# Performance work log

Measured on AMD Instinct MI355X. Metric: run time of the kernel, lower is better.

Reference implementation:

```python
import jax, jax.numpy as jnp
import numpy as np

N, E, F, HID, HEADS, L, B, R = 50000, 400000, 64, 256, 4, 4, 16, 8
C = HID // HEADS  # per-head channels = 64
LN_EPS = 1e-5
NEG_SLOPE = 0.2  # GATConv LeakyReLU default


def _posenc(n, d):
    pos = jnp.arange(n, dtype=jnp.float32)[:, None]
    i = jnp.arange(d, dtype=jnp.float32)[None, :]
    rates = 1.0 / 10000.0 ** (2.0 * jnp.floor(i / 2.0) / d)
    ang = pos * rates
    return jnp.where(jnp.arange(d)[None, :] % 2 == 0, jnp.sin(ang), jnp.cos(ang))


def _layernorm(x, g, b):
    mu = x.mean(-1, keepdims=True)
    var = ((x - mu) ** 2).mean(-1, keepdims=True)
    return (x - mu) * jax.lax.rsqrt(var + LN_EPS) * g + b


def _gat_layer(x, src, dst, W, a_src, a_dst, bias):
    # x: [N, HID]; W: [HID, HID]; a_src/a_dst: [HEADS, C]; bias: [HID]
    h = (x @ W).reshape(N, HEADS, C)
    s_src = (h * a_src[None]).sum(-1)  # [N, HEADS]
    s_dst = (h * a_dst[None]).sum(-1)  # [N, HEADS]
    e = jax.nn.leaky_relu(s_src[src] + s_dst[dst], NEG_SLOPE)  # [E', HEADS]
    m = jax.ops.segment_max(e, dst, num_segments=N)
    ex = jnp.exp(e - m[dst])
    denom = jax.ops.segment_sum(ex, dst, num_segments=N)
    alpha = ex / denom[dst]  # softmax over incoming edges per dst node
    out = jax.ops.segment_sum(alpha[:, :, None] * h[src], dst, num_segments=N)
    return out.reshape(N, HID) + bias


def setup_inputs() -> dict:
    key = jax.random.key(0)
    ks = jax.random.split(key, 20)
    sc = 0.05
    batch = jnp.sort(jax.random.randint(ks[2], (N,), 0, B))
    return {
        "x": jax.random.normal(ks[0], (N, F), jnp.float32),
        "region_emb_w": jax.random.normal(ks[3], (R, F), jnp.float32) * sc,
        "in_proj_w": jax.random.normal(ks[4], (3 * F, HID), jnp.float32) * sc,
        "in_proj_b": jnp.zeros((HID,), jnp.float32),
        "gat_w": jax.random.normal(ks[5], (L, HID, HID), jnp.float32) * sc,
        "att_src": jax.random.normal(ks[6], (L, HEADS, C), jnp.float32) * sc,
        "att_dst": jax.random.normal(ks[7], (L, HEADS, C), jnp.float32) * sc,
        "gat_b": jnp.zeros((L, HID), jnp.float32),
        "ln_g": jnp.ones((L, HID), jnp.float32),
        "ln_b": jnp.zeros((L, HID), jnp.float32),
        "ro_w1": jax.random.normal(ks[8], (HID, HID), jnp.float32) * sc,
        "ro_b1": jnp.zeros((HID,), jnp.float32),
        "ro_w2": jax.random.normal(ks[9], (HID, HID), jnp.float32) * sc,
        "ro_b2": jnp.zeros((HID,), jnp.float32),
        "edge_index": jax.random.randint(ks[1], (2, E), 0, N),
        "batch": batch,
        "region_ids": jax.random.randint(ks[10], (N,), 0, R),
    }


def reference(x, region_emb_w, in_proj_w, in_proj_b, gat_w, att_src, att_dst,
              gat_b, ln_g, ln_b, ro_w1, ro_b1, ro_w2, ro_b2,
              edge_index, batch, region_ids):
    # input features: x | region embedding | sinusoidal posenc  -> [N, 3F]
    feats = jnp.concatenate([x, region_emb_w[region_ids], _posenc(N, F)], axis=-1)
    h = feats @ in_proj_w + in_proj_b
    # add self loops once (GATConv add_self_loops=True)
    loop = jnp.arange(N)
    src = jnp.concatenate([edge_index[0], loop])
    dst = jnp.concatenate([edge_index[1], loop])
    for l in range(L):
        h = _gat_layer(h, src, dst, gat_w[l], att_src[l], att_dst[l], gat_b[l])
        h = _layernorm(jax.nn.relu(h), ln_g[l], ln_b[l])
        # dropout is identity in eval mode
    # global mean pool over graphs
    sums = jax.ops.segment_sum(h, batch, num_segments=B)
    cnts = jax.ops.segment_sum(jnp.ones((N,), h.dtype), batch, num_segments=B)
    pooled = sums / jnp.maximum(cnts, 1.0)[:, None]  # [B, HID]
    out = jax.nn.gelu(pooled @ ro_w1 + ro_b1, approximate=False) @ ro_w2 + ro_b2
    return out
```

## Files before the change

### kernel.cpp

```cpp
#include <hip/hip_runtime.h>
#include <cmath>

typedef unsigned short u16;
typedef unsigned char u8;
typedef unsigned int u32;
typedef short bf16x8 __attribute__((ext_vector_type(8)));
typedef float f32x4 __attribute__((ext_vector_type(4)));
typedef float f32x2 __attribute__((ext_vector_type(2)));

#define NN 50000
#define MP 50048
#define EE 400000
#define ET 450000
#define HIDD 256
#define KIN 192
#define LN_EPSF 1e-5f

__device__ __forceinline__ float bf2f(u16 u){ return __uint_as_float(((u32)u)<<16); }
__device__ __forceinline__ u16 f2bf(float f){
  u32 x = __float_as_uint(f);
  u32 r = x + 0x7fffu + ((x>>16)&1u);
  return (u16)(r>>16);
}
__device__ __forceinline__ u32 pack2(float a, float b){ return (u32)f2bf(a) | ((u32)f2bf(b)<<16); }
__device__ __forceinline__ u8 f2fp8(float v){
  return (u8)(__builtin_amdgcn_cvt_pk_fp8_f32(v, v, 0, false) & 0xff);
}

__device__ __forceinline__ void dma16(const u16* g, u16* lds){
  __builtin_amdgcn_global_load_lds(
      (const __attribute__((address_space(1))) void*)g,
      (__attribute__((address_space(3))) void*)lds, 16, 0, 0);
}

__global__ __launch_bounds__(256) void k_setup(
    const float* __restrict__ x, const float* __restrict__ remb, const int* __restrict__ rid,
    u16* __restrict__ feats,
    const float* __restrict__ ipw, const float* __restrict__ gatw,
    u16* __restrict__ wtin, u16* __restrict__ wtl,
    const float* __restrict__ asrc, const float* __restrict__ adst, u16* __restrict__ vmat,
    const int* __restrict__ ei, int* __restrict__ deg)
{
  int b = blockIdx.x;
  if (b < 12512){
    int e = b*768 + threadIdx.x;
    #pragma unroll
    for (int it=0; it<3; ++it, e+=256){
      int n = e / 192;
      int c = e - n*192;
      if (n >= MP) break;
      float v = 0.f;
      if (n < NN){
        if (c < 64){
          v = x[n*64 + c];
        } else if (c < 128){
          v = remb[rid[n]*64 + (c-64)];
        } else {
          int i = c - 128;
          float rate = exp2f(-(float)(2*(i>>1)) * (1.0f/64.0f) * 13.287712379549449f);
          float s, cc;
          __sincosf((float)n * rate, &s, &cc);
          v = (i & 1) ? cc : s;
        }
      }
      feats[(size_t)n*192 + c] = f2bf(v);
    }
  } else if (b < 13728){
    int idx = (b - 12512)*256 + threadIdx.x;
    if (idx < 49152){
      int n = idx / 192, k = idx - n*192;
      wtin[idx] = f2bf(ipw[k*256 + n]);
    } else {
      int j = idx - 49152;
      if (j < 262144){
        int l = j >> 16, rem = j & 65535;
        int n = rem >> 8, k = rem & 255;
        wtl[j] = f2bf(gatw[l*65536 + k*256 + n]);
      }
    }
  } else if (b < 13792){
    int idx = (b - 13728)*256 + threadIdx.x;
    if (idx < 16384){
      int l = idx >> 12, rem = idx & 4095, v = rem >> 8, k = rem & 255;
      float s = 0.f;
      if (v < 8){
        const float* a = (v < 4) ? (asrc + l*256 + v*64) : (adst + l*256 + (v-4)*64);
        const float* w = gatw + (size_t)l*65536 + k*256 + (v & 3)*64;
        #pragma unroll 8
        for (int c=0;c<64;++c) s += w[c]*a[c];
      }
      vmat[idx] = f2bf(s);
    }
  } else {
    int i = (b - 13792)*256 + threadIdx.x;
    if (i < ET){
      int d = (i < EE) ? ei[EE + i] : (i - EE);
      atomicAdd(&deg[d], 1);
    }
  }
}

__global__ void k_scan1(const int* __restrict__ deg, int* __restrict__ row_off, int* __restrict__ part){
  __shared__ int s[256];
  int n = blockIdx.x*256 + threadIdx.x;
  int v = (n < NN) ? deg[n] : 0;
  s[threadIdx.x] = v;
  __syncthreads();
  for (int off=1; off<256; off<<=1){
    int t = (threadIdx.x >= off) ? s[threadIdx.x - off] : 0;
    __syncthreads();
    s[threadIdx.x] += t;
    __syncthreads();
  }
  if (n < NN) row_off[n] = s[threadIdx.x] - v;
  if (threadIdx.x == 255) part[blockIdx.x] = s[255];
}

__global__ void k_scan23(int* __restrict__ row_off, const int* __restrict__ part, int nparts){
  __shared__ int sp[256];
  int t = threadIdx.x;
  sp[t] = (t < nparts && t < (int)blockIdx.x) ? part[t] : 0;
  __syncthreads();
  for (int off=128; off; off>>=1){
    if (t < off) sp[t] += sp[t+off];
    __syncthreads();
  }
  int n = blockIdx.x*256 + t;
  if (n < NN) row_off[n] += sp[0];
}

__global__ void k_scatter(const int* __restrict__ ei, const int* __restrict__ row_off,
                          int* __restrict__ cur, int* __restrict__ csr_src){
  int i = blockIdx.x*blockDim.x + threadIdx.x;
  if (i >= ET) return;
  int s, d;
  if (i < EE){ s = ei[i]; d = ei[EE + i]; } else { s = i - EE; d = i - EE; }
  int pos = row_off[d] + atomicAdd(&cur[d], 1);
  csr_src[pos] = s;
}

template<int K>
__global__ __launch_bounds__(256, 3) void k_gemm(
    const u16* __restrict__ A, const u16* __restrict__ Wt,
    const float* __restrict__ bias, const u16* __restrict__ vmat,
    float* __restrict__ ss, float* __restrict__ sd,
    u16* __restrict__ C, u8* __restrict__ C8, int M)
{
  __shared__ u16 Asl[2][128*32];
  __shared__ u16 Bsl[2][128*32];
  int tid = threadIdx.x;
  int wave = tid >> 6, lane = tid & 63, quad = lane >> 4, lm = lane & 15;
  int r0 = blockIdx.x * 128;
  int cb = blockIdx.y;
  int rW = (wave >> 1) * 64;
  int cW = (wave & 1) * 64;
  bool doScore = vmat && (cb == 0) && ((wave & 1) == 0);

  f32x4 acc[4][4] = {};
  f32x4 accs[4] = {};

  auto stage = [&](int buf, int k0){
    for (int m = wave; m < 8; m += 4){
      int s = m*64 + lane;
      int r = s >> 2, p = s & 3;
      int c = p ^ ((r >> 2) & 3);
      dma16(A + (size_t)(r0 + r)*K + k0 + c*8, &Asl[buf][m*512]);
    }
    for (int m = wave; m < 8; m += 4){
      int s = m*64 + lane;
      int r = s >> 2, p = s & 3;
      int c = p ^ ((r >> 2) & 3);
      dma16(Wt + (size_t)(cb*128 + r)*K + k0 + c*8, &Bsl[buf][m*512]);
    }
  };

  stage(0, 0);
  __syncthreads();

  for (int ks = 0; ks < K/32; ++ks){
    int cur = ks & 1;
    if (ks + 1 < K/32) stage(cur ^ 1, (ks+1)*32);

    bf16x8 a[4], b[4];
    #pragma unroll
    for (int i=0;i<4;++i){
      int row = rW + i*16 + lm;
      int slot = row*4 + (quad ^ ((row >> 2) & 3));
      a[i] = *(const bf16x8*)(&Asl[cur][slot*8]);
    }
    #pragma unroll
    for (int j=0;j<4;++j){
      int row = cW + j*16 + lm;
      int slot = row*4 + (quad ^ ((row >> 2) & 3));
      b[j] = *(const bf16x8*)(&Bsl[cur][slot*8]);
    }
    #pragma unroll
    for (int i=0;i<4;++i)
      #pragma unroll
      for (int j=0;j<4;++j)
        acc[i][j] = __builtin_amdgcn_mfma_f32_16x16x32_bf16(a[i], b[j], acc[i][j], 0, 0, 0);
    if (doScore){
      bf16x8 bs = *(const bf16x8*)(vmat + (size_t)lm*K + ks*32 + quad*8);
      #pragma unroll
      for (int i=0;i<4;++i)
        accs[i] = __builtin_amdgcn_mfma_f32_16x16x32_bf16(a[i], bs, accs[i], 0, 0, 0);
    }
    __syncthreads();
  }

  if (doScore){
    #pragma unroll
    for (int i=0;i<4;++i){
      #pragma unroll
      for (int r=0;r<4;++r){
        int row = r0 + rW + i*16 + quad*4 + r;
        if (row < M){
          if (lm < 4)      ss[row*4 + lm]     = accs[i][r];
          else if (lm < 8) sd[row*4 + lm - 4] = accs[i][r];
        }
      }
    }
  }

  #pragma unroll
  for (int i=0;i<4;++i){
    #pragma unroll
    for (int r=0;r<4;++r){
      int row = r0 + rW + i*16 + quad*4 + r;
      if (row < M){
        #pragma unroll
        for (int j=0;j<4;++j){
          int col = cb*128 + cW + j*16 + lm;
          float v = acc[i][j][r];
          if (bias) v += bias[col];
          if (C)  C[(size_t)row*256 + col] = f2bf(v);
          if (C8) C8[(size_t)row*256 + col] = f2fp8(v);
        }
      }
    }
  }
}

__global__ __launch_bounds__(256) void k_aggregate(
    const u8* __restrict__ h8, const float* __restrict__ ssrc, const float* __restrict__ sdst,
    const int* __restrict__ row_off, const int* __restrict__ deg, const int* __restrict__ csr_src,
    const float* __restrict__ bias, const float* __restrict__ g, const float* __restrict__ bb,
    u16* __restrict__ hout, u8* __restrict__ hout8)
{
  int wv = (blockIdx.x*blockDim.x + threadIdx.x) >> 6;
  int lane = threadIdx.x & 63;
  int half = lane >> 5;
  int hl = lane & 31;
  int n = wv*2 + half;
  if (n >= NN) return;
  int c0 = hl*8;
  int head = hl >> 3;
  float sdh = sdst[n*4 + head];
  int ro = row_off[n];
  int dg = deg[n];
  float denA = 0.f, denB = 0.f;
  float a0=0,a1=0,a2=0,a3=0,a4=0,a5=0,a6=0,a7=0;
  float b0=0,b1=0,b2=0,b3=0,b4=0,b5=0,b6=0,b7=0;
  int j = 0;
  for (; j + 2 <= dg; j += 2){
    int sA = csr_src[ro+j];
    int sB = csr_src[ro+j+1];
    uint2 uA = *(const uint2*)(h8 + (size_t)sA*HIDD + c0);
    uint2 uB = *(const uint2*)(h8 + (size_t)sB*HIDD + c0);
    float eA = ssrc[sA*4+head] + sdh;
    float eB = ssrc[sB*4+head] + sdh;
    eA = (eA > 0.f) ? eA : 0.2f*eA;
    eB = (eB > 0.f) ? eB : 0.2f*eB;
    float xA = __expf(eA), xB = __expf(eB);
    denA += xA; denB += xB;
    f32x2 pA0 = __builtin_amdgcn_cvt_pk_f32_fp8((int)uA.x, false);
    f32x2 pA1 = __builtin_amdgcn_cvt_pk_f32_fp8((int)uA.x, true);
    f32x2 pA2 = __builtin_amdgcn_cvt_pk_f32_fp8((int)uA.y, false);
    f32x2 pA3 = __builtin_amdgcn_cvt_pk_f32_fp8((int)uA.y, true);
    f32x2 pB0 = __builtin_amdgcn_cvt_pk_f32_fp8((int)uB.x, false);
    f32x2 pB1 = __builtin_amdgcn_cvt_pk_f32_fp8((int)uB.x, true);
    f32x2 pB2 = __builtin_amdgcn_cvt_pk_f32_fp8((int)uB.y, false);
    f32x2 pB3 = __builtin_amdgcn_cvt_pk_f32_fp8((int)uB.y, true);
    a0 += xA*pA0.x; a1 += xA*pA0.y; a2 += xA*pA1.x; a3 += xA*pA1.y;
    a4 += xA*pA2.x; a5 += xA*pA2.y; a6 += xA*pA3.x; a7 += xA*pA3.y;
    b0 += xB*pB0.x; b1 += xB*pB0.y; b2 += xB*pB1.x; b3 += xB*pB1.y;
    b4 += xB*pB2.x; b5 += xB*pB2.y; b6 += xB*pB3.x; b7 += xB*pB3.y;
  }
  if (j < dg){
    int sA = csr_src[ro+j];
    uint2 uA = *(const uint2*)(h8 + (size_t)sA*HIDD + c0);
    float eA = ssrc[sA*4+head] + sdh;
    eA = (eA > 0.f) ? eA : 0.2f*eA;
    float xA = __expf(eA);
    denA += xA;
    f32x2 pA0 = __builtin_amdgcn_cvt_pk_f32_fp8((int)uA.x, false);
    f32x2 pA1 = __builtin_amdgcn_cvt_pk_f32_fp8((int)uA.x, true);
    f32x2 pA2 = __builtin_amdgcn_cvt_pk_f32_fp8((int)uA.y, false);
    f32x2 pA3 = __builtin_amdgcn_cvt_pk_f32_fp8((int)uA.y, true);
    a0 += xA*pA0.x; a1 += xA*pA0.y; a2 += xA*pA1.x; a3 += xA*pA1.y;
    a4 += xA*pA2.x; a5 += xA*pA2.y; a6 += xA*pA3.x; a7 += xA*pA3.y;
  }
  float inv = 1.f / (denA + denB);
  float y[8];
  y[0]=a0+b0; y[1]=a1+b1; y[2]=a2+b2; y[3]=a3+b3;
  y[4]=a4+b4; y[5]=a5+b5; y[6]=a6+b6; y[7]=a7+b7;
  float4 bi0 = *(const float4*)(bias + c0);
  float4 bi1 = *(const float4*)(bias + c0 + 4);
  y[0]=fmaxf(y[0]*inv+bi0.x,0.f); y[1]=fmaxf(y[1]*inv+bi0.y,0.f);
  y[2]=fmaxf(y[2]*inv+bi0.z,0.f); y[3]=fmaxf(y[3]*inv+bi0.w,0.f);
  y[4]=fmaxf(y[4]*inv+bi1.x,0.f); y[5]=fmaxf(y[5]*inv+bi1.y,0.f);
  y[6]=fmaxf(y[6]*inv+bi1.z,0.f); y[7]=fmaxf(y[7]*inv+bi1.w,0.f);
  float sum = (y[0]+y[1])+(y[2]+y[3])+((y[4]+y[5])+(y[6]+y[7]));
  #pragma unroll
  for (int o=16;o>=1;o>>=1) sum += __shfl_xor(sum, o);
  float mu = sum * (1.f/256.f);
  float d[8], sq = 0.f;
  #pragma unroll
  for (int k=0;k<8;++k){ d[k] = y[k]-mu; sq += d[k]*d[k]; }
  #pragma unroll
  for (int o=16;o>=1;o>>=1) sq += __shfl_xor(sq, o);
  float rs = rsqrtf(sq*(1.f/256.f) + LN_EPSF);
  float4 g0 = *(const float4*)(g + c0);
  float4 g1 = *(const float4*)(g + c0 + 4);
  float4 q0 = *(const float4*)(bb + c0);
  float4 q1 = *(const float4*)(bb + c0 + 4);
  float o0 = d[0]*rs*g0.x + q0.x, o1 = d[1]*rs*g0.y + q0.y;
  float o2 = d[2]*rs*g0.z + q0.z, o3 = d[3]*rs*g0.w + q0.w;
  float o4v= d[4]*rs*g1.x + q1.x, o5 = d[5]*rs*g1.y + q1.y;
  float o6 = d[6]*rs*g1.z + q1.z, o7 = d[7]*rs*g1.w + q1.w;
  if (hout8){
    u32 w0 = (u32)__builtin_amdgcn_cvt_pk_fp8_f32(o0, o1, 0, false);
    w0 = (u32)__builtin_amdgcn_cvt_pk_fp8_f32(o2, o3, (int)w0, true);
    u32 w1 = (u32)__builtin_amdgcn_cvt_pk_fp8_f32(o4v, o5, 0, false);
    w1 = (u32)__builtin_amdgcn_cvt_pk_fp8_f32(o6, o7, (int)w1, true);
    uint2 o8; o8.x = w0; o8.y = w1;
    *(uint2*)(hout8 + (size_t)n*HIDD + c0) = o8;
  } else {
    uint4 o4;
    o4.x = pack2(o0, o1);
    o4.y = pack2(o2, o3);
    o4.z = pack2(o4v, o5);
    o4.w = pack2(o6, o7);
    *(uint4*)(hout + (size_t)n*HIDD + c0) = o4;
  }
}

__global__ __launch_bounds__(256) void k_pool(
    const u8* __restrict__ h8, const int* __restrict__ batch,
    float* __restrict__ pooled, float* __restrict__ cnt)
{
  const int chunk = 25;
  int t = threadIdx.x;
  int n0 = blockIdx.x*chunk;
  int n1 = min(n0 + chunk, NN);
  if (n0 >= n1) return;
  float acc = 0.f;
  int curb = batch[n0];
  int runStart = n0;
  bool hi = (t & 2) != 0;
  for (int n=n0; n<n1; ++n){
    int b = batch[n];
    if (b != curb){
      atomicAdd(&pooled[curb*HIDD + t], acc);
      if (t == 0) atomicAdd(&cnt[curb], (float)(n - runStart));
      acc = 0.f; curb = b; runStart = n;
    }
    u32 w = *(const u32*)(h8 + (size_t)n*HIDD + (t & ~3));
    f32x2 p = hi ? __builtin_amdgcn_cvt_pk_f32_fp8((int)w, true)
                 : __builtin_amdgcn_cvt_pk_f32_fp8((int)w, false);
    acc += (t & 1) ? p.y : p.x;
  }
  atomicAdd(&pooled[curb*HIDD + t], acc);
  if (t == 0) atomicAdd(&cnt[curb], (float)(n1 - runStart));
}

__global__ __launch_bounds__(256) void k_readout(
    const float* __restrict__ pooled, const float* __restrict__ cnt,
    const float* __restrict__ w1, const float* __restrict__ b1,
    const float* __restrict__ w2, const float* __restrict__ b2,
    float* __restrict__ out)
{
  __shared__ float p[256], mid[256];
  int b = blockIdx.x, t = threadIdx.x;
  float c = fmaxf(cnt[b], 1.f);
  p[t] = pooled[b*HIDD + t] / c;
  __syncthreads();
  float acc = b1[t];
  for (int k=0;k<256;++k) acc += p[k]*w1[k*256+t];
  mid[t] = 0.5f*acc*(1.f + erff(acc*0.70710678118654752f));
  __syncthreads();
  float acc2 = b2[t];
  for (int k=0;k<256;++k) acc2 += mid[k]*w2[k*256+t];
  out[b*HIDD + t] = acc2;
}

extern "C" void kernel_launch(void* const* d_in, const int* in_sizes, int n_in,
                              void* d_out, int out_size, void* d_ws, size_t ws_size,
                              hipStream_t stream)
{
  const float* x    = (const float*)d_in[0];
  const float* remb = (const float*)d_in[1];
  const float* ipw  = (const float*)d_in[2];
  const float* ipb  = (const float*)d_in[3];
  const float* gatw = (const float*)d_in[4];
  const float* asrc = (const float*)d_in[5];
  const float* adst = (const float*)d_in[6];
  const float* gatb = (const float*)d_in[7];
  const float* lng  = (const float*)d_in[8];
  const float* lnb  = (const float*)d_in[9];
  const float* row1 = (const float*)d_in[10];
  const float* rob1 = (const float*)d_in[11];
  const float* row2 = (const float*)d_in[12];
  const float* rob2 = (const float*)d_in[13];
  const int* ei   = (const int*)d_in[14];
  const int* batch= (const int*)d_in[15];
  const int* rid  = (const int*)d_in[16];

  char* ws = (char*)d_ws;
  int*   deg  = (int*)  (ws + 0);
  int*   cur  = (int*)  (ws + 200192);
  float* cnt  = (float*)(ws + 400384);
  float* pool = (float*)(ws + 400640);
  int*   row  = (int*)  (ws + 417024);
  int*   part = (int*)  (ws + 617216);
  int*   csr  = (int*)  (ws + 618240);
  float* ss   = (float*)(ws + 2418432);
  float* sd   = (float*)(ws + 3219200);
  u16*   vmat = (u16*)  (ws + 4019968);
  u16*   feats= (u16*)  (ws + 4052736);
  u16*   wtin = (u16*)  (ws + 23271168);
  u16*   wtl  = (u16*)  (ws + 23369472);
  u16*   hA   = (u16*)  (ws + 23893760);
  u8*    hA8  = (u8*)   (ws + 23893760);
  u8*    hB8  = (u8*)   (ws + 49518336);

  (void)hipMemsetAsync(ws, 0, 417024, stream);

  k_setup <<<15550, 256, 0, stream>>>(x, remb, rid, feats, ipw, gatw, wtin, wtl,
                                      asrc, adst, vmat, ei, deg);
  k_scan1 <<<196, 256, 0, stream>>>(deg, row, part);
  k_scan23<<<196, 256, 0, stream>>>(row, part, 196);
  k_scatter<<<1758, 256, 0, stream>>>(ei, row, cur, csr);

  k_gemm<KIN><<<dim3(391,2), 256, 0, stream>>>(feats, wtin, ipb, nullptr,
                                               nullptr, nullptr, hA, nullptr, NN);

  for (int l = 0; l < 4; ++l){
    k_gemm<HIDD><<<dim3(391,2), 256, 0, stream>>>(hA, wtl + (size_t)l*HIDD*HIDD, nullptr,
                                                  vmat + (size_t)l*16*256, ss, sd,
                                                  nullptr, hB8, NN);
    if (l < 3){
      k_aggregate<<<6250, 256, 0, stream>>>(hB8, ss, sd, row, deg, csr,
                                            gatb + l*HIDD, lng + l*HIDD, lnb + l*HIDD,
                                            hA, nullptr);
    } else {
      k_aggregate<<<6250, 256, 0, stream>>>(hB8, ss, sd, row, deg, csr,
                                            gatb + l*HIDD, lng + l*HIDD, lnb + l*HIDD,
                                            nullptr, hA8);
    }
  }

  k_pool   <<<2000, 256, 0, stream>>>(hA8, batch, pool, cnt);
  k_readout<<<16, 256, 0, stream>>>(pool, cnt, row1, rob1, row2, rob2, (float*)d_out);
}
```

Measured before the change: 470.4 us.

## Vectorize feature build, software-pipeline edge gathers, and halve pool blocks

The feature setup is split into three block ranges (raw x, region embedding, positional encoding). Each thread now writes 8 bf16 values with 128-bit stores instead of computing one scalar element at a time. The aggregation loop is software-pipelined: the next pair of edge indices, fp8 rows and source scores are loaded before the current pair is processed, to hide gather latency. The pooling chunk is doubled so half as many blocks issue atomics, which adds more serial work per block.

After: 456.0 us. -3.0%, faster.

```diff
diff --git a/kernel.cpp b/kernel.cpp
--- a/kernel.cpp
+++ b/kernel.cpp
@@ -42,31 +42,53 @@
     const int* __restrict__ ei, int* __restrict__ deg)
 {
   int b = blockIdx.x;
-  if (b < 12512){
-    int e = b*768 + threadIdx.x;
-    #pragma unroll
-    for (int it=0; it<3; ++it, e+=256){
-      int n = e / 192;
-      int c = e - n*192;
-      if (n >= MP) break;
-      float v = 0.f;
-      if (n < NN){
-        if (c < 64){
-          v = x[n*64 + c];
-        } else if (c < 128){
-          v = remb[rid[n]*64 + (c-64)];
-        } else {
-          int i = c - 128;
-          float rate = exp2f(-(float)(2*(i>>1)) * (1.0f/64.0f) * 13.287712379549449f);
-          float s, cc;
-          __sincosf((float)n * rate, &s, &cc);
-          v = (i & 1) ? cc : s;
-        }
+  if (b < 1564){
+    int u = b*256 + threadIdx.x;
+    int n = u >> 3;
+    int c0 = (u & 7) * 8;
+    uint4 o = {0u,0u,0u,0u};
+    if (n < NN){
+      const float* xp = x + (size_t)n*64 + c0;
+      float4 v0 = *(const float4*)xp;
+      float4 v1 = *(const float4*)(xp + 4);
+      o.x = pack2(v0.x, v0.y); o.y = pack2(v0.z, v0.w);
+      o.z = pack2(v1.x, v1.y); o.w = pack2(v1.z, v1.w);
+    }
+    *(uint4*)(feats + (size_t)n*192 + c0) = o;
+  } else if (b < 3128){
+    int u = (b-1564)*256 + threadIdx.x;
+    int n = u >> 3;
+    int c0 = (u & 7) * 8;
+    uint4 o = {0u,0u,0u,0u};
+    if (n < NN){
+      const float* rp = remb + (size_t)rid[n]*64 + c0;
+      float4 v0 = *(const float4*)rp;
+      float4 v1 = *(const float4*)(rp + 4);
+      o.x = pack2(v0.x, v0.y); o.y = pack2(v0.z, v0.w);
+      o.z = pack2(v1.x, v1.y); o.w = pack2(v1.z, v1.w);
+    }
+    *(uint4*)(feats + (size_t)n*192 + 64 + c0) = o;
+  } else if (b < 4692){
+    int u = (b-3128)*256 + threadIdx.x;
+    int n = u >> 3;
+    int i0 = (u & 7) * 8;
+    uint4 o = {0u,0u,0u,0u};
+    if (n < NN){
+      float fn = (float)n;
+      float os[8];
+      #pragma unroll
+      for (int m=0;m<4;++m){
+        float rate = exp2f(-(float)(i0 + 2*m) * (1.0f/64.0f) * 13.287712379549449f);
+        float s, c;
+        __sincosf(fn * rate, &s, &c);
+        os[2*m] = s; os[2*m+1] = c;
       }
-      feats[(size_t)n*192 + c] = f2bf(v);
-    }
-  } else if (b < 13728){
-    int idx = (b - 12512)*256 + threadIdx.x;
+      o.x = pack2(os[0], os[1]); o.y = pack2(os[2], os[3]);
+      o.z = pack2(os[4], os[5]); o.w = pack2(os[6], os[7]);
+    }
+    *(uint4*)(feats + (size_t)n*192 + 128 + i0) = o;
+  } else if (b < 5908){
+    int idx = (b - 4692)*256 + threadIdx.x;
     if (idx < 49152){
       int n = idx / 192, k = idx - n*192;
       wtin[idx] = f2bf(ipw[k*256 + n]);
@@ -78,8 +100,8 @@
         wtl[j] = f2bf(gatw[l*65536 + k*256 + n]);
       }
     }
-  } else if (b < 13792){
-    int idx = (b - 13728)*256 + threadIdx.x;
+  } else if (b < 5972){
+    int idx = (b - 5908)*256 + threadIdx.x;
     if (idx < 16384){
       int l = idx >> 12, rem = idx & 4095, v = rem >> 8, k = rem & 255;
       float s = 0.f;
@@ -92,7 +114,7 @@
       vmat[idx] = f2bf(s);
     }
   } else {
-    int i = (b - 13792)*256 + threadIdx.x;
+    int i = (b - 5972)*256 + threadIdx.x;
     if (i < ET){
       int d = (i < EE) ? ei[EE + i] : (i - EE);
       atomicAdd(&deg[d], 1);
@@ -261,35 +283,24 @@
   float denA = 0.f, denB = 0.f;
   float a0=0,a1=0,a2=0,a3=0,a4=0,a5=0,a6=0,a7=0;
   float b0=0,b1=0,b2=0,b3=0,b4=0,b5=0,b6=0,b7=0;
-  int j = 0;
-  for (; j + 2 <= dg; j += 2){
-    int sA = csr_src[ro+j];
-    int sB = csr_src[ro+j+1];
-    uint2 uA = *(const uint2*)(h8 + (size_t)sA*HIDD + c0);
-    uint2 uB = *(const uint2*)(h8 + (size_t)sB*HIDD + c0);
-    float eA = ssrc[sA*4+head] + sdh;
-    float eB = ssrc[sB*4+head] + sdh;
-    eA = (eA > 0.f) ? eA : 0.2f*eA;
-    eB = (eB > 0.f) ? eB : 0.2f*eB;
-    float xA = __expf(eA), xB = __expf(eB);
-    denA += xA; denB += xB;
-    f32x2 pA0 = __builtin_amdgcn_cvt_pk_f32_fp8((int)uA.x, false);
-    f32x2 pA1 = __builtin_amdgcn_cvt_pk_f32_fp8((int)uA.x, true);
-    f32x2 pA2 = __builtin_amdgcn_cvt_pk_f32_fp8((int)uA.y, false);
-    f32x2 pA3 = __builtin_amdgcn_cvt_pk_f32_fp8((int)uA.y, true);
-    f32x2 pB0 = __builtin_amdgcn_cvt_pk_f32_fp8((int)uB.x, false);
-    f32x2 pB1 = __builtin_amdgcn_cvt_pk_f32_fp8((int)uB.x, true);
-    f32x2 pB2 = __builtin_amdgcn_cvt_pk_f32_fp8((int)uB.y, false);
-    f32x2 pB3 = __builtin_amdgcn_cvt_pk_f32_fp8((int)uB.y, true);
-    a0 += xA*pA0.x; a1 += xA*pA0.y; a2 += xA*pA1.x; a3 += xA*pA1.y;
-    a4 += xA*pA2.x; a5 += xA*pA2.y; a6 += xA*pA3.x; a7 += xA*pA3.y;
-    b0 += xB*pB0.x; b1 += xB*pB0.y; b2 += xB*pB1.x; b3 += xB*pB1.y;
-    b4 += xB*pB2.x; b5 += xB*pB2.y; b6 += xB*pB3.x; b7 += xB*pB3.y;
-  }
-  if (j < dg){
-    int sA = csr_src[ro+j];
-    uint2 uA = *(const uint2*)(h8 + (size_t)sA*HIDD + c0);
-    float eA = ssrc[sA*4+head] + sdh;
+
+  int sA = csr_src[ro];
+  int sB = (1 < dg) ? csr_src[ro + 1] : 0;
+  uint2 uA = *(const uint2*)(h8 + (size_t)sA*HIDD + c0);
+  uint2 uB = *(const uint2*)(h8 + (size_t)sB*HIDD + c0);
+  float fA = ssrc[sA*4 + head];
+  float fB = ssrc[sB*4 + head];
+
+  for (int j = 0; j < dg; j += 2){
+    bool hasB = (j + 1 < dg);
+    int nA = (j + 2 < dg) ? csr_src[ro + j + 2] : 0;
+    int nB = (j + 3 < dg) ? csr_src[ro + j + 3] : 0;
+    uint2 vA = *(const uint2*)(h8 + (size_t)nA*HIDD + c0);
+    uint2 vB = *(const uint2*)(h8 + (size_t)nB*HIDD + c0);
+    float gA = ssrc[nA*4 + head];
+    float gB = ssrc[nB*4 + head];
+
+    float eA = fA + sdh;
     eA = (eA > 0.f) ? eA : 0.2f*eA;
     float xA = __expf(eA);
     denA += xA;
@@ -299,7 +310,21 @@
     f32x2 pA3 = __builtin_amdgcn_cvt_pk_f32_fp8((int)uA.y, true);
     a0 += xA*pA0.x; a1 += xA*pA0.y; a2 += xA*pA1.x; a3 += xA*pA1.y;
     a4 += xA*pA2.x; a5 += xA*pA2.y; a6 += xA*pA3.x; a7 += xA*pA3.y;
-  }
+    if (hasB){
+      float eB = fB + sdh;
+      eB = (eB > 0.f) ? eB : 0.2f*eB;
+      float xB = __expf(eB);
+      denB += xB;
+      f32x2 pB0 = __builtin_amdgcn_cvt_pk_f32_fp8((int)uB.x, false);
+      f32x2 pB1 = __builtin_amdgcn_cvt_pk_f32_fp8((int)uB.x, true);
+      f32x2 pB2 = __builtin_amdgcn_cvt_pk_f32_fp8((int)uB.y, false);
+      f32x2 pB3 = __builtin_amdgcn_cvt_pk_f32_fp8((int)uB.y, true);
+      b0 += xB*pB0.x; b1 += xB*pB0.y; b2 += xB*pB1.x; b3 += xB*pB1.y;
+      b4 += xB*pB2.x; b5 += xB*pB2.y; b6 += xB*pB3.x; b7 += xB*pB3.y;
+    }
+    sA = nA; sB = nB; uA = vA; uB = vB; fA = gA; fB = gB;
+  }
+
   float inv = 1.f / (denA + denB);
   float y[8];
   y[0]=a0+b0; y[1]=a1+b1; y[2]=a2+b2; y[3]=a3+b3;
@@ -349,7 +374,7 @@
     const u8* __restrict__ h8, const int* __restrict__ batch,
     float* __restrict__ pooled, float* __restrict__ cnt)
 {
-  const int chunk = 25;
+  const int chunk = 50;
   int t = threadIdx.x;
   int n0 = blockIdx.x*chunk;
   int n1 = min(n0 + chunk, NN);
@@ -436,8 +461,8 @@
 
   (void)hipMemsetAsync(ws, 0, 417024, stream);
 
-  k_setup <<<15550, 256, 0, stream>>>(x, remb, rid, feats, ipw, gatw, wtin, wtl,
-                                      asrc, adst, vmat, ei, deg);
+  k_setup <<<7730, 256, 0, stream>>>(x, remb, rid, feats, ipw, gatw, wtin, wtl,
+                                     asrc, adst, vmat, ei, deg);
   k_scan1 <<<196, 256, 0, stream>>>(deg, row, part);
   k_scan23<<<196, 256, 0, stream>>>(row, part, 196);
   k_scatter<<<1758, 256, 0, stream>>>(ei, row, cur, csr);
@@ -460,6 +485,6 @@
     }
   }
 
-  k_pool   <<<2000, 256, 0, stream>>>(hA8, batch, pool, cnt);
+  k_pool   <<<1000, 256, 0, stream>>>(hA8, batch, pool, cnt);
   k_readout<<<16, 256, 0, stream>>>(pool, cnt, row1, rob1, row2, rob2, (float*)d_out);
 }
```
